# Performance work log

Measured on AMD Instinct MI355X. Metric: run time of the kernel, lower is better.

Reference implementation:

```python
import jax, jax.numpy as jnp
import numpy as np
import math

B, S, D, H = 4, 2048, 1024, 16
DH = D // H  # per-head dim = 64
MASK_VAL = -1000000.0


def setup_inputs() -> dict:
    key = jax.random.key(0)
    ks = jax.random.split(key, 9)
    queries = jax.random.normal(ks[0], (B, S, D), dtype=jnp.float32)
    keys = jax.random.normal(ks[1], (B, S, D), dtype=jnp.float32)
    values = jax.random.normal(ks[2], (B, S, D), dtype=jnp.float32)
    valid_lens = jax.random.randint(ks[3], (B,), 0, S, dtype=jnp.int32)
    scale = 1.0 / math.sqrt(D)
    Wq = jax.random.normal(ks[4], (D, D), dtype=jnp.float32) * scale
    Wk = jax.random.normal(ks[5], (D, D), dtype=jnp.float32) * scale
    Wv = jax.random.normal(ks[6], (D, D), dtype=jnp.float32) * scale
    Wo = jax.random.normal(ks[7], (D, D), dtype=jnp.float32) * scale
    return {"queries": queries, "keys": keys, "values": values,
            "valid_lens": valid_lens, "Wq": Wq, "Wk": Wk, "Wv": Wv, "Wo": Wo}


def _split_heads(x):  # [B,S,D] -> [B,H,S,DH]
    b, s, _ = x.shape
    return x.reshape(b, s, H, DH).transpose(0, 2, 1, 3)


def reference(queries, keys, values, valid_lens, Wq, Wk, Wv, Wo):
    q = _split_heads(queries @ Wq)  # [B,H,S,DH]
    k = _split_heads(keys @ Wk)
    v = _split_heads(values @ Wv)
    scores = jnp.einsum('bhqd,bhkd->bhqk', q, k) / jnp.sqrt(jnp.float32(DH))
    # mask key positions >= valid_len[b] (sequence_mask with value=-1e6)
    key_pos = jnp.arange(S)  # [S]
    mask = key_pos[None, None, None, :] < valid_lens[:, None, None, None]  # [B,1,1,S]
    scores = jnp.where(mask, scores, MASK_VAL)
    attn = jax.nn.softmax(scores, axis=-1)  # [B,H,S,S] -- the 1GB intermediate
    out = jnp.einsum('bhqk,bhkd->bhqd', attn, v)  # [B,H,S,DH]
    out = out.transpose(0, 2, 1, 3).reshape(B, S, D)  # concat heads
    return out @ Wo
```

## Files before the change

kernel.cpp:

```cpp
#include <hip/hip_runtime.h>

#define BB 4
#define SS 2048
#define DD 1024
#define HH 16
#define DHH 64

typedef _Float16 half8 __attribute__((ext_vector_type(8)));
typedef _Float16 half4v __attribute__((ext_vector_type(4)));
typedef float floatx4 __attribute__((ext_vector_type(4)));

#define GLOBAL_AS __attribute__((address_space(1)))
#define LDS_AS __attribute__((address_space(3)))

__global__ void wt_kernel(const float* __restrict__ w0, const float* __restrict__ w1,
                          const float* __restrict__ w2, const float* __restrict__ w3,
                          _Float16* __restrict__ wt) {
  __shared__ float tile[32][33];
  int z = blockIdx.z;
  const float* w = (z == 0) ? w0 : (z == 1) ? w1 : (z == 2) ? w2 : w3;
  _Float16* dst = wt + (size_t)z * 1024 * 1024;
  int k0 = blockIdx.x * 32, n0 = blockIdx.y * 32;
  int tx = threadIdx.x & 31, ty = threadIdx.x >> 5;
#pragma unroll
  for (int r = ty; r < 32; r += 8) tile[r][tx] = w[(size_t)(k0 + r) * 1024 + n0 + tx];
  __syncthreads();
#pragma unroll
  for (int r = ty; r < 32; r += 8) dst[(size_t)(n0 + r) * 1024 + k0 + tx] = (_Float16)tile[tx][r];
}

__global__ void cvt3_kernel(const float* __restrict__ q, const float* __restrict__ k,
                            const float* __restrict__ v, _Float16* __restrict__ dst) {
  int z = blockIdx.y;
  const float* src = (z == 0) ? q : (z == 1) ? k : v;
  size_t i = ((size_t)blockIdx.x * 256 + threadIdx.x) * 8;
  float4 f0 = *(const float4*)(src + i);
  float4 f1 = *(const float4*)(src + i + 4);
  half8 h = {(_Float16)f0.x, (_Float16)f0.y, (_Float16)f0.z, (_Float16)f0.w,
             (_Float16)f1.x, (_Float16)f1.y, (_Float16)f1.z, (_Float16)f1.w};
  *(half8*)(dst + (size_t)z * 8388608 + i) = h;
}

__global__ __launch_bounds__(256) void qkv_gemm(const _Float16* __restrict__ Acat,
                                                const _Float16* __restrict__ Wt,
                                                _Float16* __restrict__ Qf,
                                                _Float16* __restrict__ Kf,
                                                _Float16* __restrict__ Vt) {
  __shared__ _Float16 lA[128 * 32];
  __shared__ _Float16 lB[128 * 32];
  int tid = threadIdx.x;
  int wave = tid >> 6, lane = tid & 63, quad = lane >> 4, l15 = lane & 15;
  int bn = blockIdx.x, bm = blockIdx.y;
  int proj = bm >> 6;
  int wm = wave >> 1, wn = wave & 1;

  const _Float16* A = Acat + (size_t)bm * 128 * 1024;
  const _Float16* W = Wt + (size_t)proj * 1024 * 1024;

  floatx4 fzero = {0.f, 0.f, 0.f, 0.f};
  floatx4 acc[4][4];
#pragma unroll
  for (int i = 0; i < 4; ++i)
#pragma unroll
    for (int j = 0; j < 4; ++j) acc[i][j] = fzero;

  int g0 = tid, g1 = 256 + tid;
  int row0 = g0 >> 2, gc0 = (g0 & 3) ^ ((row0 >> 1) & 3);
  int row1 = g1 >> 2, gc1 = (g1 & 3) ^ ((row1 >> 1) & 3);
  const _Float16* a0 = A + ((size_t)row0 * 1024 + gc0 * 8);
  const _Float16* a1 = A + ((size_t)row1 * 1024 + gc1 * 8);
  const _Float16* b0 = W + ((size_t)(bn * 128 + row0) * 1024 + gc0 * 8);
  const _Float16* b1 = W + ((size_t)(bn * 128 + row1) * 1024 + gc1 * 8);

  for (int k0 = 0; k0 < 1024; k0 += 32) {
    __builtin_amdgcn_global_load_lds((const GLOBAL_AS void*)(a0 + k0),
                                     (LDS_AS void*)(lA + g0 * 8), 16, 0, 0);
    __builtin_amdgcn_global_load_lds((const GLOBAL_AS void*)(a1 + k0),
                                     (LDS_AS void*)(lA + g1 * 8), 16, 0, 0);
    __builtin_amdgcn_global_load_lds((const GLOBAL_AS void*)(b0 + k0),
                                     (LDS_AS void*)(lB + g0 * 8), 16, 0, 0);
    __builtin_amdgcn_global_load_lds((const GLOBAL_AS void*)(b1 + k0),
                                     (LDS_AS void*)(lB + g1 * 8), 16, 0, 0);
    __syncthreads();

    half8 af[4], bf[4];
#pragma unroll
    for (int i = 0; i < 4; ++i) {
      int row = wm * 64 + i * 16 + l15;
      af[i] = *(const half8*)(lA + (row * 4 + (quad ^ ((row >> 1) & 3))) * 8);
    }
#pragma unroll
    for (int j = 0; j < 4; ++j) {
      int row = wn * 64 + j * 16 + l15;
      bf[j] = *(const half8*)(lB + (row * 4 + (quad ^ ((row >> 1) & 3))) * 8);
    }
#pragma unroll
    for (int i = 0; i < 4; ++i)
#pragma unroll
      for (int j = 0; j < 4; ++j)
        acc[i][j] = __builtin_amdgcn_mfma_f32_16x16x32_f16(af[i], bf[j], acc[i][j], 0, 0, 0);
    __syncthreads();
  }

  int rloc = (bm & 63) * 128;
#pragma unroll
  for (int i = 0; i < 4; ++i) {
#pragma unroll
    for (int j = 0; j < 4; ++j) {
      int rowb = rloc + wm * 64 + i * 16 + quad * 4;
      int col = bn * 128 + wn * 64 + j * 16 + l15;
      if (proj == 0) {
#pragma unroll
        for (int r = 0; r < 4; ++r)
          Qf[(size_t)(rowb + r) * 1024 + col] = (_Float16)(acc[i][j][r] * 0.125f);
      } else if (proj == 1) {
#pragma unroll
        for (int r = 0; r < 4; ++r)
          Kf[(size_t)(rowb + r) * 1024 + col] = (_Float16)acc[i][j][r];
      } else {
        int b = rowb >> 11, s = rowb & 2047;
        half4v pk = {(_Float16)acc[i][j][0], (_Float16)acc[i][j][1],
                     (_Float16)acc[i][j][2], (_Float16)acc[i][j][3]};
        *(half4v*)(Vt + (size_t)(b * 1024 + col) * 2048 + s) = pk;
      }
    }
  }
}

__global__ __launch_bounds__(256) void gemm_out(const _Float16* __restrict__ A,
                                                const _Float16* __restrict__ Wt,
                                                float* __restrict__ C) {
  __shared__ _Float16 lA[128 * 32];
  __shared__ _Float16 lB[128 * 32];
  int tid = threadIdx.x;
  int wave = tid >> 6, lane = tid & 63, quad = lane >> 4, l15 = lane & 15;
  int bn = blockIdx.x, bm = blockIdx.y;
  int wm = wave >> 1, wn = wave & 1;

  floatx4 fzero = {0.f, 0.f, 0.f, 0.f};
  floatx4 acc[4][4];
#pragma unroll
  for (int i = 0; i < 4; ++i)
#pragma unroll
    for (int j = 0; j < 4; ++j) acc[i][j] = fzero;

  int g0 = tid, g1 = 256 + tid;
  int row0 = g0 >> 2, gc0 = (g0 & 3) ^ ((row0 >> 1) & 3);
  int row1 = g1 >> 2, gc1 = (g1 & 3) ^ ((row1 >> 1) & 3);
  const _Float16* a0 = A + ((size_t)(bm * 128 + row0) * 1024 + gc0 * 8);
  const _Float16* a1 = A + ((size_t)(bm * 128 + row1) * 1024 + gc1 * 8);
  const _Float16* b0 = Wt + ((size_t)(bn * 128 + row0) * 1024 + gc0 * 8);
  const _Float16* b1 = Wt + ((size_t)(bn * 128 + row1) * 1024 + gc1 * 8);

  for (int k0 = 0; k0 < 1024; k0 += 32) {
    __builtin_amdgcn_global_load_lds((const GLOBAL_AS void*)(a0 + k0),
                                     (LDS_AS void*)(lA + g0 * 8), 16, 0, 0);
    __builtin_amdgcn_global_load_lds((const GLOBAL_AS void*)(a1 + k0),
                                     (LDS_AS void*)(lA + g1 * 8), 16, 0, 0);
    __builtin_amdgcn_global_load_lds((const GLOBAL_AS void*)(b0 + k0),
                                     (LDS_AS void*)(lB + g0 * 8), 16, 0, 0);
    __builtin_amdgcn_global_load_lds((const GLOBAL_AS void*)(b1 + k0),
                                     (LDS_AS void*)(lB + g1 * 8), 16, 0, 0);
    __syncthreads();

    half8 af[4], bf[4];
#pragma unroll
    for (int i = 0; i < 4; ++i) {
      int row = wm * 64 + i * 16 + l15;
      af[i] = *(const half8*)(lA + (row * 4 + (quad ^ ((row >> 1) & 3))) * 8);
    }
#pragma unroll
    for (int j = 0; j < 4; ++j) {
      int row = wn * 64 + j * 16 + l15;
      bf[j] = *(const half8*)(lB + (row * 4 + (quad ^ ((row >> 1) & 3))) * 8);
    }
#pragma unroll
    for (int i = 0; i < 4; ++i)
#pragma unroll
      for (int j = 0; j < 4; ++j)
        acc[i][j] = __builtin_amdgcn_mfma_f32_16x16x32_f16(af[i], bf[j], acc[i][j], 0, 0, 0);
    __syncthreads();
  }

#pragma unroll
  for (int i = 0; i < 4; ++i)
#pragma unroll
    for (int j = 0; j < 4; ++j) {
      int rowb = bm * 128 + wm * 64 + i * 16 + quad * 4;
      int col = bn * 128 + wn * 64 + j * 16 + l15;
#pragma unroll
      for (int r = 0; r < 4; ++r) C[(size_t)(rowb + r) * 1024 + col] = acc[i][j][r];
    }
}

__global__ __launch_bounds__(256) void attn_kernel(const _Float16* __restrict__ Q,
                                                   const _Float16* __restrict__ K,
                                                   const _Float16* __restrict__ Vt,
                                                   const int* __restrict__ vlens,
                                                   _Float16* __restrict__ O) {
  __shared__ _Float16 lK[64 * 64];
  __shared__ _Float16 lV[64 * 64];
  __shared__ _Float16 lP[4 * 16 * 64];

  int tid = threadIdx.x, wave = tid >> 6, lane = tid & 63, quad = lane >> 4, l15 = lane & 15;
  int bh = blockIdx.y, b = bh >> 4, h = bh & 15;
  int q0 = blockIdx.x * 64;
  int vlen = vlens[b];
  int nch = (vlen == 0) ? (SS / 64) : ((vlen + 63) >> 6);
  float mask_val = (vlen == 0) ? 0.0f : -1.0e6f;

  const _Float16* qb = Q + ((size_t)(b * SS + q0 + wave * 16 + l15) * DD + h * 64 + quad * 8);
  half8 qf0 = *(const half8*)qb;
  half8 qf1 = *(const half8*)(qb + 32);

  float l_part[4] = {0.f, 0.f, 0.f, 0.f};
  floatx4 fzero = {0.f, 0.f, 0.f, 0.f};
  floatx4 o[4];
#pragma unroll
  for (int j = 0; j < 4; ++j) o[j] = fzero;

  for (int kc = 0; kc < nch; ++kc) {
    int kb = kc * 64;
#pragma unroll
    for (int ss = tid; ss < 512; ss += 256) {
      int row = ss >> 3, gc = ss & 7;
      int sidx = (row * 8 + (gc ^ (row & 7))) * 8;
      *(half8*)(lK + sidx) =
          *(const half8*)(K + ((size_t)(b * SS + kb + row) * DD + h * 64 + gc * 8));
      *(half8*)(lV + sidx) =
          *(const half8*)(Vt + ((size_t)(b * DD + h * 64 + row) * SS + kb + gc * 8));
    }
    __syncthreads();

    floatx4 sacc[4];
#pragma unroll
    for (int j = 0; j < 4; ++j) sacc[j] = fzero;
#pragma unroll
    for (int ks = 0; ks < 2; ++ks) {
      half8 qf = ks ? qf1 : qf0;
#pragma unroll
      for (int j = 0; j < 4; ++j) {
        int row = j * 16 + l15, gc = ks * 4 + quad;
        half8 kf = *(const half8*)(lK + (row * 8 + (gc ^ (row & 7))) * 8);
        sacc[j] = __builtin_amdgcn_mfma_f32_16x16x32_f16(qf, kf, sacc[j], 0, 0, 0);
      }
    }

    bool clean = (kb + 64 <= vlen);
#pragma unroll
    for (int j = 0; j < 4; ++j) {
      int key = kb + j * 16 + l15;
      bool valid = clean | (key < vlen);
#pragma unroll
      for (int r = 0; r < 4; ++r) {
        float s = valid ? sacc[j][r] : mask_val;
        float p = __expf(s);
        l_part[r] += p;
        int row = quad * 4 + r, col = j * 16 + l15;
        int gc = col >> 3, off = col & 7;
        lP[wave * 1024 + row * 64 + (gc ^ (row & 7)) * 8 + off] = (_Float16)p;
      }
    }

#pragma unroll
    for (int ks = 0; ks < 2; ++ks) {
      int gc = ks * 4 + quad;
      half8 pf = *(const half8*)(lP + wave * 1024 + l15 * 64 + (gc ^ (l15 & 7)) * 8);
#pragma unroll
      for (int j = 0; j < 4; ++j) {
        int row = j * 16 + l15;
        half8 vf = *(const half8*)(lV + (row * 8 + (gc ^ (row & 7))) * 8);
        o[j] = __builtin_amdgcn_mfma_f32_16x16x32_f16(pf, vf, o[j], 0, 0, 0);
      }
    }
    __syncthreads();
  }

  float inv_l[4];
#pragma unroll
  for (int r = 0; r < 4; ++r) {
    float l = l_part[r];
#pragma unroll
    for (int off = 1; off < 16; off <<= 1) l += __shfl_xor(l, off);
    inv_l[r] = 1.0f / l;
  }
#pragma unroll
  for (int j = 0; j < 4; ++j) {
    int col = h * 64 + j * 16 + l15;
#pragma unroll
    for (int r = 0; r < 4; ++r) {
      int qrow = q0 + wave * 16 + quad * 4 + r;
      O[(size_t)(b * SS + qrow) * DD + col] = (_Float16)(o[j][r] * inv_l[r]);
    }
  }
}

extern "C" void kernel_launch(void* const* d_in, const int* in_sizes, int n_in,
                              void* d_out, int out_size, void* d_ws, size_t ws_size,
                              hipStream_t stream) {
  const float* q = (const float*)d_in[0];
  const float* k = (const float*)d_in[1];
  const float* v = (const float*)d_in[2];
  const int* vl = (const int*)d_in[3];
  const float* wq = (const float*)d_in[4];
  const float* wk = (const float*)d_in[5];
  const float* wv = (const float*)d_in[6];
  const float* wo = (const float*)d_in[7];

  char* ws = (char*)d_ws;
  _Float16* Wt = (_Float16*)ws;
  _Float16* Acat = (_Float16*)(ws + (8u << 20));
  _Float16* Qf = (_Float16*)(ws + (56u << 20));
  _Float16* Kf = (_Float16*)(ws + (72u << 20));
  _Float16* Vt = (_Float16*)(ws + (88u << 20));
  _Float16* Of = Acat;

  dim3 blk(256);

  wt_kernel<<<dim3(32, 32, 4), blk, 0, stream>>>(wq, wk, wv, wo, Wt);
  cvt3_kernel<<<dim3(4096, 3), blk, 0, stream>>>(q, k, v, Acat);
  qkv_gemm<<<dim3(8, 192), blk, 0, stream>>>(Acat, Wt, Qf, Kf, Vt);
  attn_kernel<<<dim3(32, 64), blk, 0, stream>>>(Qf, Kf, Vt, vl, Of);
  gemm_out<<<dim3(8, 64), blk, 0, stream>>>(Of, Wt + (3u << 20), (float*)d_out);
}
```

Measured before the change: 340.6 us.

## Transpose score MFMA, pack P writes, and use exp2 with prescaled Q

```diff
diff --git a/kernel.cpp b/kernel.cpp
--- a/kernel.cpp
+++ b/kernel.cpp
@@ -8,10 +8,13 @@
 
 typedef _Float16 half8 __attribute__((ext_vector_type(8)));
 typedef _Float16 half4v __attribute__((ext_vector_type(4)));
+typedef _Float16 half2v __attribute__((ext_vector_type(2)));
 typedef float floatx4 __attribute__((ext_vector_type(4)));
 
 #define GLOBAL_AS __attribute__((address_space(1)))
 #define LDS_AS __attribute__((address_space(3)))
+
+#define QSCALE 0.18033688011112042f
 
 __global__ void wt_kernel(const float* __restrict__ w0, const float* __restrict__ w1,
                           const float* __restrict__ w2, const float* __restrict__ w3,
@@ -112,7 +115,7 @@
       if (proj == 0) {
 #pragma unroll
         for (int r = 0; r < 4; ++r)
-          Qf[(size_t)(rowb + r) * 1024 + col] = (_Float16)(acc[i][j][r] * 0.125f);
+          Qf[(size_t)(rowb + r) * 1024 + col] = (_Float16)(acc[i][j][r] * QSCALE);
       } else if (proj == 1) {
 #pragma unroll
         for (int r = 0; r < 4; ++r)
@@ -213,7 +216,23 @@
   half8 qf0 = *(const half8*)qb;
   half8 qf1 = *(const half8*)(qb + 32);
 
-  float l_part[4] = {0.f, 0.f, 0.f, 0.f};
+  int off[2][4];
+#pragma unroll
+  for (int ks = 0; ks < 2; ++ks)
+#pragma unroll
+    for (int j = 0; j < 4; ++j) {
+      int row = j * 16 + l15, gc = ks * 4 + quad;
+      off[ks][j] = (row * 8 + (gc ^ (row & 7))) * 8;
+    }
+  int m = (l15 & 7) << 1;
+  int pbase = wave * 1024 + l15 * 64;
+  int wp[4], rp[2];
+#pragma unroll
+  for (int j = 0; j < 4; ++j) wp[j] = pbase + (((j * 4 + quad) ^ m) << 2);
+#pragma unroll
+  for (int ks = 0; ks < 2; ++ks) rp[ks] = pbase + (((ks * 8 + quad * 2) ^ m) << 2);
+
+  float l_acc = 0.f;
   floatx4 fzero = {0.f, 0.f, 0.f, 0.f};
   floatx4 o[4];
 #pragma unroll
@@ -240,57 +259,63 @@
       half8 qf = ks ? qf1 : qf0;
 #pragma unroll
       for (int j = 0; j < 4; ++j) {
-        int row = j * 16 + l15, gc = ks * 4 + quad;
-        half8 kf = *(const half8*)(lK + (row * 8 + (gc ^ (row & 7))) * 8);
-        sacc[j] = __builtin_amdgcn_mfma_f32_16x16x32_f16(qf, kf, sacc[j], 0, 0, 0);
+        half8 kf = *(const half8*)(lK + off[ks][j]);
+        sacc[j] = __builtin_amdgcn_mfma_f32_16x16x32_f16(kf, qf, sacc[j], 0, 0, 0);
       }
     }
 
-    bool clean = (kb + 64 <= vlen);
-#pragma unroll
-    for (int j = 0; j < 4; ++j) {
-      int key = kb + j * 16 + l15;
-      bool valid = clean | (key < vlen);
-#pragma unroll
-      for (int r = 0; r < 4; ++r) {
-        float s = valid ? sacc[j][r] : mask_val;
-        float p = __expf(s);
-        l_part[r] += p;
-        int row = quad * 4 + r, col = j * 16 + l15;
-        int gc = col >> 3, off = col & 7;
-        lP[wave * 1024 + row * 64 + (gc ^ (row & 7)) * 8 + off] = (_Float16)p;
-      }
+    float p[4][4];
+    if (kb + 64 <= vlen) {
+#pragma unroll
+      for (int j = 0; j < 4; ++j)
+#pragma unroll
+        for (int r = 0; r < 4; ++r) p[j][r] = __builtin_amdgcn_exp2f(sacc[j][r]);
+    } else {
+#pragma unroll
+      for (int j = 0; j < 4; ++j)
+#pragma unroll
+        for (int r = 0; r < 4; ++r) {
+          int key = kb + j * 16 + quad * 4 + r;
+          float s = (key < vlen) ? sacc[j][r] : mask_val;
+          p[j][r] = __builtin_amdgcn_exp2f(s);
+        }
+    }
+
+#pragma unroll
+    for (int j = 0; j < 4; ++j) {
+      l_acc += (p[j][0] + p[j][1]) + (p[j][2] + p[j][3]);
+      half2v lo = __builtin_bit_cast(half2v, __builtin_amdgcn_cvt_pkrtz(p[j][0], p[j][1]));
+      half2v hi = __builtin_bit_cast(half2v, __builtin_amdgcn_cvt_pkrtz(p[j][2], p[j][3]));
+      half4v w4 = {lo.x, lo.y, hi.x, hi.y};
+      *(half4v*)(lP + wp[j]) = w4;
     }
 
 #pragma unroll
     for (int ks = 0; ks < 2; ++ks) {
-      int gc = ks * 4 + quad;
-      half8 pf = *(const half8*)(lP + wave * 1024 + l15 * 64 + (gc ^ (l15 & 7)) * 8);
+      half8 pf = *(const half8*)(lP + rp[ks]);
 #pragma unroll
       for (int j = 0; j < 4; ++j) {
-        int row = j * 16 + l15;
-        half8 vf = *(const half8*)(lV + (row * 8 + (gc ^ (row & 7))) * 8);
+        half8 vf = *(const half8*)(lV + off[ks][j]);
         o[j] = __builtin_amdgcn_mfma_f32_16x16x32_f16(pf, vf, o[j], 0, 0, 0);
       }
     }
     __syncthreads();
   }
 
-  float inv_l[4];
-#pragma unroll
-  for (int r = 0; r < 4; ++r) {
-    float l = l_part[r];
-#pragma unroll
-    for (int off = 1; off < 16; off <<= 1) l += __shfl_xor(l, off);
-    inv_l[r] = 1.0f / l;
-  }
+  float l = l_acc;
+  l += __shfl_xor(l, 16);
+  l += __shfl_xor(l, 32);
+  float inv = 1.0f / l;
+  float inv_r[4];
+#pragma unroll
+  for (int r = 0; r < 4; ++r) inv_r[r] = __shfl(inv, quad * 4 + r);
 #pragma unroll
   for (int j = 0; j < 4; ++j) {
     int col = h * 64 + j * 16 + l15;
 #pragma unroll
     for (int r = 0; r < 4; ++r) {
       int qrow = q0 + wave * 16 + quad * 4 + r;
-      O[(size_t)(b * SS + qrow) * DD + col] = (_Float16)(o[j][r] * inv_l[r]);
+      O[(size_t)(b * SS + qrow) * DD + col] = (_Float16)(o[j][r] * inv_r[r]);
     }
   }
 }
```

Result: no change. 338.9 us (-0.5%).
